# Kernel tuning notes

Measured on AMD Instinct MI355X. Metric: run time of the kernel, lower is better.

## Reference

```python
import jax, jax.numpy as jnp
import numpy as np

NUM_HEADS = 16
HEAD_DIM = 128  # d_out / num_heads = 2048 / 16
WINDOW = 2048   # sliding_window_size


def setup_inputs() -> dict:
    key = jax.random.key(0)
    kx, kq, kk, kv, ko = jax.random.split(key, 5)
    b, s, d = 2, 2048, 2048
    scale = 0.02
    return {
        "x": jax.random.normal(kx, (b, s, d), dtype=jnp.float32),
        "Wq": jax.random.normal(kq, (d, d), dtype=jnp.float32) * scale,
        "Wk": jax.random.normal(kk, (d, d), dtype=jnp.float32) * scale,
        "Wv": jax.random.normal(kv, (d, d), dtype=jnp.float32) * scale,
        "Wo": jax.random.normal(ko, (d, d), dtype=jnp.float32) * scale,
    }


def reference(x, Wq, Wk, Wv, Wo):
    b, s, _ = x.shape
    H, Dh, W = NUM_HEADS, HEAD_DIM, WINDOW

    # qkv projections (no bias), split into heads: [b, s, H, Dh]
    q = (x @ Wq).reshape(b, s, H, Dh)
    k = (x @ Wk).reshape(b, s, H, Dh)
    v = (x @ Wv).reshape(b, s, H, Dh)

    # attn scores: [b, H, q, k]
    scores = jnp.einsum("bqhd,bkhd->bhqk", q, k)

    # sliding-window mask from absolute positions (fresh cache: q_start=k_start=0)
    pos = jnp.arange(s)
    diff = pos[:, None] - pos[None, :]  # q_pos - k_pos
    mask = (diff < 0) | (diff >= W)
    scores = jnp.where(mask[None, None], -jnp.inf, scores)

    attn = jax.nn.softmax(scores / np.sqrt(Dh).astype(np.float32), axis=-1)

    # context: [b, s, H, Dh] -> [b, s, d_out]
    ctx = jnp.einsum("bhqk,bkhd->bqhd", attn, v).reshape(b, s, H * Dh)
    return ctx @ Wo
```

## Files before the change

### kernel.cpp

```cpp
#include <hip/hip_runtime.h>

typedef __bf16 bf16;
typedef __bf16 bf16x4 __attribute__((ext_vector_type(4)));
typedef __bf16 bf16x8 __attribute__((ext_vector_type(8)));
typedef float f32x4 __attribute__((ext_vector_type(4)));

#define B_ 2
#define S_ 2048
#define D_ 2048
#define H_ 16
#define DH_ 128
#define QKVN 6144

__device__ __forceinline__ void async_load16(const bf16* g, bf16* l) {
    __builtin_amdgcn_global_load_lds((const __attribute__((address_space(1))) void*)g,
                                     (__attribute__((address_space(3))) void*)l, 16, 0, 0);
}

__device__ __forceinline__ unsigned int bf16_bits(float x) {
    bf16 h = (bf16)x;
    return (unsigned int)__builtin_bit_cast(unsigned short, h);
}

__global__ __launch_bounds__(256) void cvt_kernel(const float* __restrict__ src,
                                                  bf16* __restrict__ dst) {
    size_t i = (size_t)blockIdx.x * 256 + threadIdx.x;
    const float4* s = (const float4*)src;
    float4 a = s[2 * i], b = s[2 * i + 1];
    bf16x8 o;
    o[0] = (bf16)a.x; o[1] = (bf16)a.y; o[2] = (bf16)a.z; o[3] = (bf16)a.w;
    o[4] = (bf16)b.x; o[5] = (bf16)b.y; o[6] = (bf16)b.z; o[7] = (bf16)b.w;
    *(bf16x8*)(dst + 8 * i) = o;
}

__global__ __launch_bounds__(256) void wtrans_kernel(const float* __restrict__ Wq,
                                                     const float* __restrict__ Wk,
                                                     const float* __restrict__ Wv,
                                                     const float* __restrict__ Wo,
                                                     bf16* __restrict__ WqkvT,
                                                     bf16* __restrict__ WoT) {
    __shared__ unsigned int tile[64][65];
    int z = blockIdx.z;
    const float* src = (z == 0) ? Wq : (z == 1) ? Wk : (z == 2) ? Wv : Wo;
    bf16* dst = (z < 3) ? (WqkvT + (size_t)z * D_ * D_) : WoT;
    int r0 = blockIdx.y * 64, c0 = blockIdx.x * 64;
    int t = threadIdx.x;
    int tr = t >> 4, tc4 = (t & 15) * 4;
#pragma unroll
    for (int it = 0; it < 4; ++it) {
        int r = it * 16 + tr;
        float4 v = *(const float4*)(src + (size_t)(r0 + r) * D_ + c0 + tc4);
        tile[r][tc4 + 0] = bf16_bits(v.x);
        tile[r][tc4 + 1] = bf16_bits(v.y);
        tile[r][tc4 + 2] = bf16_bits(v.z);
        tile[r][tc4 + 3] = bf16_bits(v.w);
    }
    __syncthreads();
#pragma unroll
    for (int it = 0; it < 4; ++it) {
        int a = it * 16 + tr;
        unsigned u0 = tile[tc4 + 0][a], u1 = tile[tc4 + 1][a];
        unsigned u2 = tile[tc4 + 2][a], u3 = tile[tc4 + 3][a];
        uint2 v;
        v.x = (u0 & 0xffffu) | (u1 << 16);
        v.y = (u2 & 0xffffu) | (u3 << 16);
        *(uint2*)(dst + (size_t)(c0 + a) * D_ + r0 + tc4) = v;
    }
}

__global__ __launch_bounds__(256) void vtrans_kernel(const bf16* __restrict__ qkv,
                                                     bf16* __restrict__ vt) {
    __shared__ unsigned int tile[64][65];
    int bh = blockIdx.z;
    int b = bh >> 4, h = bh & 15;
    int s0 = blockIdx.x * 64, d0 = blockIdx.y * 64;
    int t = threadIdx.x, tr = t >> 4, tc4 = (t & 15) * 4;
#pragma unroll
    for (int it = 0; it < 4; ++it) {
        int r = it * 16 + tr;
        uint2 v = *(const uint2*)(qkv + (size_t)(b * S_ + s0 + r) * QKVN + 2 * D_ + h * DH_ + d0 + tc4);
        tile[r][tc4 + 0] = v.x & 0xffffu;
        tile[r][tc4 + 1] = v.x >> 16;
        tile[r][tc4 + 2] = v.y & 0xffffu;
        tile[r][tc4 + 3] = v.y >> 16;
    }
    __syncthreads();
#pragma unroll
    for (int it = 0; it < 4; ++it) {
        int a = it * 16 + tr;
        unsigned u0 = tile[tc4 + 0][a], u1 = tile[tc4 + 1][a];
        unsigned u2 = tile[tc4 + 2][a], u3 = tile[tc4 + 3][a];
        uint2 v;
        v.x = (u0 & 0xffffu) | (u1 << 16);
        v.y = (u2 & 0xffffu) | (u3 << 16);
        *(uint2*)(vt + (size_t)bh * DH_ * S_ + (size_t)(d0 + a) * S_ + s0 + tc4) = v;
    }
}

template <typename CT>
__global__ __launch_bounds__(256) void gemm_bt(const bf16* __restrict__ A,
                                               const bf16* __restrict__ Bt,
                                               CT* __restrict__ C,
                                               int M, int N, int K) {
    __shared__ __align__(16) bf16 As[128 * 32];
    __shared__ __align__(16) bf16 Bs[128 * 32];
    int t = threadIdx.x;
    int w = t >> 6, l = t & 63;
    int quad = l >> 4, lr = l & 15;
    int wr = w >> 1, wc = w & 1;
    size_t m0 = (size_t)blockIdx.y * 128, n0 = (size_t)blockIdx.x * 128;
    int srow = l >> 2, scol = (l & 3) * 8;

    f32x4 acc[4][4];
#pragma unroll
    for (int i = 0; i < 4; ++i)
#pragma unroll
        for (int j = 0; j < 4; ++j) acc[i][j] = (f32x4){0.f, 0.f, 0.f, 0.f};

    for (int k0 = 0; k0 < K; k0 += 32) {
        __syncthreads();
#pragma unroll
        for (int i = 0; i < 2; ++i) {
            int c = w * 2 + i;
            async_load16(A + (m0 + c * 16 + srow) * (size_t)K + k0 + scol, As + c * 512);
            async_load16(Bt + (n0 + c * 16 + srow) * (size_t)K + k0 + scol, Bs + c * 512);
        }
        asm volatile("s_waitcnt vmcnt(0)" ::: "memory");
        __syncthreads();
        bf16x8 af[4], bfr[4];
#pragma unroll
        for (int i = 0; i < 4; ++i) af[i] = *(const bf16x8*)(As + (wr * 64 + i * 16 + lr) * 32 + quad * 8);
#pragma unroll
        for (int j = 0; j < 4; ++j) bfr[j] = *(const bf16x8*)(Bs + (wc * 64 + j * 16 + lr) * 32 + quad * 8);
#pragma unroll
        for (int i = 0; i < 4; ++i)
#pragma unroll
            for (int j = 0; j < 4; ++j)
                acc[i][j] = __builtin_amdgcn_mfma_f32_16x16x32_bf16(af[i], bfr[j], acc[i][j], 0, 0, 0);
    }

    size_t bm = m0 + wr * 64 + quad * 4;
    size_t bn = n0 + wc * 64 + lr;
#pragma unroll
    for (int i = 0; i < 4; ++i)
#pragma unroll
        for (int j = 0; j < 4; ++j)
#pragma unroll
            for (int r = 0; r < 4; ++r)
                C[(bm + i * 16 + r) * (size_t)N + bn + j * 16] = (CT)acc[i][j][r];
}

__global__ __launch_bounds__(128) void attn_kernel(const bf16* __restrict__ qkv,
                                                   const bf16* __restrict__ vt,
                                                   bf16* __restrict__ ctx) {
    __shared__ __align__(16) bf16 Ks[2][64 * 128];
    __shared__ __align__(16) bf16 Vts[2][128 * 64];
    __shared__ __align__(16) bf16 Ps[2][32][68];

    int y = blockIdx.y;
    int p = blockIdx.x;
    int b = y >> 4, h = y & 15;
    int t = threadIdx.x, w = t >> 6, l = t & 63;
    int quad = l >> 4, lr = l & 15;

    const bf16* qbase = qkv + (size_t)b * S_ * QKVN + h * DH_;
    const bf16* kbase = qbase + D_;
    const bf16* vbase = vt + (size_t)y * DH_ * S_;

    const int qtA = p, qtB = 31 - p;
    const int nA = p + 1;

    auto stage = [&](int kt, int bi) {
#pragma unroll
        for (int ii = 0; ii < 8; ++ii) {
            int i = 8 * w + ii;
            int row = 4 * i + (l >> 4);
            int cl = (l & 15) ^ (row & 7);
            async_load16(kbase + (size_t)(kt * 64 + row) * QKVN + cl * 8, Ks[bi] + i * 512);
        }
#pragma unroll
        for (int ii = 0; ii < 8; ++ii) {
            int i = 8 * w + ii;
            int dh = 8 * i + (l >> 3);
            int cl = (l & 7) ^ (dh & 7);
            async_load16(vbase + (size_t)dh * S_ + kt * 64 + cl * 8, Vts[bi] + i * 512);
        }
    };

    const float sc2 = 0.12751745f;

    int qt = qtA, q0 = qt * 64;
    bf16x8 qf[2][4];
    auto loadQ = [&]() {
#pragma unroll
        for (int g = 0; g < 2; ++g)
#pragma unroll
            for (int kk = 0; kk < 4; ++kk) {
                bf16x8 raw = *(const bf16x8*)(qbase + (size_t)(q0 + w * 32 + g * 16 + lr) * QKVN + kk * 32 + quad * 8);
#pragma unroll
                for (int e = 0; e < 8; ++e) qf[g][kk][e] = (bf16)((float)raw[e] * sc2);
            }
    };
    loadQ();

    float L_r[2][4];
    f32x4 o[2][8];
#pragma unroll
    for (int g = 0; g < 2; ++g) {
#pragma unroll
        for (int r = 0; r < 4; ++r) L_r[g][r] = 0.f;
#pragma unroll
        for (int nt = 0; nt < 8; ++nt) o[g][nt] = (f32x4){0.f, 0.f, 0.f, 0.f};
    }

    auto epilogue = [&](int q0e) {
#pragma unroll
        for (int g = 0; g < 2; ++g) {
#pragma unroll
            for (int d = 1; d < 16; d <<= 1)
#pragma unroll
                for (int r = 0; r < 4; ++r) L_r[g][r] += __shfl_xor(L_r[g][r], d, 64);
#pragma unroll
            for (int r = 0; r < 4; ++r) {
                float inv = __builtin_amdgcn_rcpf(L_r[g][r]);
                int q = q0e + w * 32 + g * 16 + quad * 4 + r;
#pragma unroll
                for (int nt = 0; nt < 8; ++nt)
                    ctx[(size_t)(b * S_ + q) * D_ + h * DH_ + nt * 16 + lr] = (bf16)(o[g][nt][r] * inv);
            }
        }
    };

    stage(0, 0);

    for (int it = 0; it < 33; ++it) {
        int buf = it & 1;
        asm volatile("s_waitcnt vmcnt(0)" ::: "memory");
        __syncthreads();
        if (it + 1 < 33) {
            int nit = it + 1;
            int nkt = (nit < nA) ? nit : (nit - nA);
            stage(nkt, buf ^ 1);
        }
        int kt = (it < nA) ? it : (it - nA);

        f32x4 s[2][4];
#pragma unroll
        for (int g = 0; g < 2; ++g)
#pragma unroll
            for (int jt = 0; jt < 4; ++jt) s[g][jt] = (f32x4){0.f, 0.f, 0.f, 0.f};
#pragma unroll
        for (int kk = 0; kk < 4; ++kk)
#pragma unroll
            for (int jt = 0; jt < 4; ++jt) {
                bf16x8 kf = *(const bf16x8*)(Ks[buf] + (jt * 16 + lr) * 128 + ((4 * kk + quad) ^ (lr & 7)) * 8);
                s[0][jt] = __builtin_amdgcn_mfma_f32_16x16x32_bf16(qf[0][kk], kf, s[0][jt], 0, 0, 0);
                s[1][jt] = __builtin_amdgcn_mfma_f32_16x16x32_bf16(qf[1][kk], kf, s[1][jt], 0, 0, 0);
            }

        bool diag = (kt == qt);
#pragma unroll
        for (int g = 0; g < 2; ++g) {
#pragma unroll
            for (int jt = 0; jt < 4; ++jt) {
                int keyi = jt * 16 + lr;
#pragma unroll
                for (int r = 0; r < 4; ++r) {
                    float s2 = s[g][jt][r];
                    if (diag && keyi > w * 32 + g * 16 + quad * 4 + r) s2 = -3.0e38f;
                    float pv = __builtin_amdgcn_exp2f(s2);
                    s[g][jt][r] = pv;
                    L_r[g][r] += pv;
                }
            }
#pragma unroll
            for (int jt = 0; jt < 4; ++jt)
#pragma unroll
                for (int r = 0; r < 4; ++r)
                    Ps[w][g * 16 + quad * 4 + r][jt * 16 + lr] = (bf16)s[g][jt][r];
        }
        asm volatile("s_waitcnt lgkmcnt(0)" ::: "memory");

#pragma unroll
        for (int ks = 0; ks < 2; ++ks) {
            bf16x8 pf[2];
#pragma unroll
            for (int g = 0; g < 2; ++g) {
                const bf16* pp = &Ps[w][g * 16 + lr][ks * 32 + quad * 8];
                bf16x4 lo = *(const bf16x4*)pp;
                bf16x4 hi = *(const bf16x4*)(pp + 4);
                pf[g] = __builtin_shufflevector(lo, hi, 0, 1, 2, 3, 4, 5, 6, 7);
            }
#pragma unroll
            for (int nt = 0; nt < 8; ++nt) {
                bf16x8 vf = *(const bf16x8*)(Vts[buf] + (nt * 16 + lr) * 64 + ((4 * ks + quad) ^ (lr & 7)) * 8);
                o[0][nt] = __builtin_amdgcn_mfma_f32_16x16x32_bf16(pf[0], vf, o[0][nt], 0, 0, 0);
                o[1][nt] = __builtin_amdgcn_mfma_f32_16x16x32_bf16(pf[1], vf, o[1][nt], 0, 0, 0);
            }
        }

        if (it == nA - 1) {
            epilogue(q0);
            qt = qtB;
            q0 = qt * 64;
            loadQ();
#pragma unroll
            for (int g = 0; g < 2; ++g) {
#pragma unroll
                for (int r = 0; r < 4; ++r) L_r[g][r] = 0.f;
#pragma unroll
                for (int nt = 0; nt < 8; ++nt) o[g][nt] = (f32x4){0.f, 0.f, 0.f, 0.f};
            }
        }
    }

    epilogue(q0);
}

extern "C" void kernel_launch(void* const* d_in, const int* in_sizes, int n_in,
                              void* d_out, int out_size, void* d_ws, size_t ws_size,
                              hipStream_t stream) {
    const float* x  = (const float*)d_in[0];
    const float* Wq = (const float*)d_in[1];
    const float* Wk = (const float*)d_in[2];
    const float* Wv = (const float*)d_in[3];
    const float* Wo = (const float*)d_in[4];
    float* out = (float*)d_out;

    char* ws = (char*)d_ws;
    bf16* WqkvT = (bf16*)(ws);
    bf16* WoT   = (bf16*)(ws + 25165824);
    bf16* qkv   = (bf16*)(ws + 33554432);
    bf16* vt    = (bf16*)(ws + 83886080);
    bf16* ctx   = (bf16*)(ws + 100663296);
    bf16* xb    = (bf16*)(ws + 117440512);

    cvt_kernel<<<4096, 256, 0, stream>>>(x, xb);
    wtrans_kernel<<<dim3(32, 32, 4), 256, 0, stream>>>(Wq, Wk, Wv, Wo, WqkvT, WoT);
    gemm_bt<bf16><<<dim3(48, 32), 256, 0, stream>>>(xb, WqkvT, qkv, B_ * S_, QKVN, D_);
    vtrans_kernel<<<dim3(32, 2, 32), 256, 0, stream>>>(qkv, vt);
    attn_kernel<<<dim3(16, 32), 128, 0, stream>>>(qkv, vt, ctx);
    gemm_bt<float><<<dim3(16, 32), 256, 0, stream>>>(ctx, WoT, out, B_ * S_, D_, D_);
}
```

Before: 417.4 us.

## Add specialized 256x256 tiled QKV GEMM with swizzled LDS and interleaved prefetch

Replaces the generic gemm_bt for the QKV projection with a dedicated 512-thread kernel computing 256x256 output tiles. It uses XOR-swizzled LDS to avoid bank conflicts, double-buffered async global-to-LDS loads interleaved with four MFMA quarter-steps, a block-index swizzle for L2 locality, and s_setprio around MFMA bursts. The goal is higher operand reuse and better overlap of loads and compute. The cost is larger shared memory use (128KB per block), many barriers, and hand-tuned waitcnt sequencing that has to be exactly right.

```diff
diff --git a/kernel.cpp b/kernel.cpp
--- a/kernel.cpp
+++ b/kernel.cpp
@@ -150,6 +150,172 @@
                 C[(bm + i * 16 + r) * (size_t)N + bn + j * 16] = (CT)acc[i][j][r];
 }
 
+#define QK_K 2048
+#define QK_N 6144
+
+__device__ __forceinline__ bf16x8 lds_frag(const bf16* tile, int row, int colByte) {
+    int off = row * 128 + (colByte ^ (((row >> 2) & 1) << 5));
+    return *(const bf16x8*)((const char*)tile + off);
+}
+
+template <int MH, int NH>
+__device__ __forceinline__ void mmaq8(f32x4 (&acc)[8][4], const bf16x8 (&afr)[4][2],
+                                      const bf16x8 (&bf)[2][2]) {
+    __builtin_amdgcn_s_setprio(1);
+#pragma unroll
+    for (int i = 0; i < 4; ++i)
+#pragma unroll
+        for (int j = 0; j < 2; ++j)
+#pragma unroll
+            for (int kk = 0; kk < 2; ++kk)
+                acc[MH * 4 + i][NH * 2 + j] = __builtin_amdgcn_mfma_f32_16x16x32_bf16(
+                    afr[i][kk], bf[j][kk], acc[MH * 4 + i][NH * 2 + j], 0, 0, 0);
+    __builtin_amdgcn_s_setprio(0);
+}
+
+__global__ __launch_bounds__(512, 2) void gemm_qkv(const bf16* __restrict__ A,
+                                                   const bf16* __restrict__ Bt,
+                                                   bf16* __restrict__ C) {
+    __shared__ __align__(16) bf16 As[2][256 * 64];
+    __shared__ __align__(16) bf16 Bs[2][256 * 64];
+
+    int t = threadIdx.x;
+    int wid = t >> 6, lane = t & 63;
+    int quad = lane >> 4, lr = lane & 15;
+    int wr = wid >> 2, wn = wid & 3;
+
+    int bid = blockIdx.x;
+    int swz = (bid & 7) * 48 + (bid >> 3);
+    int tn = swz >> 4, tm = swz & 15;
+    size_t m0 = (size_t)tm * 256, n0 = (size_t)tn * 256;
+
+    int row_r[2], c8s_r[2];
+#pragma unroll
+    for (int r = 0; r < 2; ++r) {
+        int idx = r * 512 + t;
+        row_r[r] = idx >> 3;
+        c8s_r[r] = (idx & 7) ^ (((row_r[r] >> 2) & 1) << 1);
+    }
+
+    auto stA = [&](int kt, int bufi, int h) {
+#pragma unroll
+        for (int r = 0; r < 2; ++r)
+            async_load16(A + (m0 + h * 128 + row_r[r]) * (size_t)QK_K + kt * 64 + c8s_r[r] * 8,
+                         &As[bufi][(h * 1024 + r * 512 + wid * 64) * 8]);
+    };
+    auto stB = [&](int kt, int bufi, int h) {
+#pragma unroll
+        for (int r = 0; r < 2; ++r)
+            async_load16(Bt + (n0 + h * 128 + row_r[r]) * (size_t)QK_K + kt * 64 + c8s_r[r] * 8,
+                         &Bs[bufi][(h * 1024 + r * 512 + wid * 64) * 8]);
+    };
+
+    f32x4 acc[8][4];
+#pragma unroll
+    for (int i = 0; i < 8; ++i)
+#pragma unroll
+        for (int j = 0; j < 4; ++j) acc[i][j] = (f32x4){0.f, 0.f, 0.f, 0.f};
+
+    bf16x8 afr[4][2], bf0[2][2], bf1[2][2];
+
+    auto readA = [&](int bufi, int mh) {
+#pragma unroll
+        for (int i = 0; i < 4; ++i)
+#pragma unroll
+            for (int kk = 0; kk < 2; ++kk)
+                afr[i][kk] = lds_frag(As[bufi], mh * 128 + wr * 64 + i * 16 + lr, kk * 64 + quad * 16);
+    };
+    auto readB = [&](int bufi, int nh, bf16x8 (&bf)[2][2]) {
+#pragma unroll
+        for (int j = 0; j < 2; ++j)
+#pragma unroll
+            for (int kk = 0; kk < 2; ++kk)
+                bf[j][kk] = lds_frag(Bs[bufi], nh * 128 + wn * 32 + j * 16 + lr, kk * 64 + quad * 16);
+    };
+
+    stA(0, 0, 0);
+    stB(0, 0, 0);
+    stB(0, 0, 1);
+    stA(0, 0, 1);
+    asm volatile("s_waitcnt vmcnt(4)" ::: "memory");
+    __builtin_amdgcn_s_barrier();
+
+    const int NKT = QK_K / 64;
+    for (int kt = 0; kt < NKT - 1; ++kt) {
+        int cb = kt & 1, nb = cb ^ 1;
+        readA(cb, 0);
+        readB(cb, 0, bf0);
+        stA(kt + 1, nb, 0);
+        asm volatile("s_waitcnt vmcnt(4)" ::: "memory");
+        __builtin_amdgcn_s_barrier();
+        asm volatile("s_waitcnt lgkmcnt(0)" ::: "memory");
+        __builtin_amdgcn_sched_barrier(0);
+        mmaq8<0, 0>(acc, afr, bf0);
+        __builtin_amdgcn_s_barrier();
+        readB(cb, 1, bf1);
+        stB(kt + 1, nb, 0);
+        asm volatile("s_waitcnt vmcnt(4)" ::: "memory");
+        __builtin_amdgcn_s_barrier();
+        asm volatile("s_waitcnt lgkmcnt(0)" ::: "memory");
+        __builtin_amdgcn_sched_barrier(0);
+        mmaq8<0, 1>(acc, afr, bf1);
+        __builtin_amdgcn_s_barrier();
+        readA(cb, 1);
+        stB(kt + 1, nb, 1);
+        __builtin_amdgcn_s_barrier();
+        asm volatile("s_waitcnt lgkmcnt(0)" ::: "memory");
+        __builtin_amdgcn_sched_barrier(0);
+        mmaq8<1, 0>(acc, afr, bf0);
+        __builtin_amdgcn_s_barrier();
+        stA(kt + 1, nb, 1);
+        asm volatile("s_waitcnt vmcnt(4)" ::: "memory");
+        __builtin_amdgcn_s_barrier();
+        mmaq8<1, 1>(acc, afr, bf1);
+        __builtin_amdgcn_s_barrier();
+    }
+
+    {
+        int cb = (NKT - 1) & 1;
+        readA(cb, 0);
+        readB(cb, 0, bf0);
+        asm volatile("s_waitcnt vmcnt(2)" ::: "memory");
+        __builtin_amdgcn_s_barrier();
+        asm volatile("s_waitcnt lgkmcnt(0)" ::: "memory");
+        __builtin_amdgcn_sched_barrier(0);
+        mmaq8<0, 0>(acc, afr, bf0);
+        __builtin_amdgcn_s_barrier();
+        readB(cb, 1, bf1);
+        asm volatile("s_waitcnt vmcnt(0)" ::: "memory");
+        __builtin_amdgcn_s_barrier();
+        asm volatile("s_waitcnt lgkmcnt(0)" ::: "memory");
+        __builtin_amdgcn_sched_barrier(0);
+        mmaq8<0, 1>(acc, afr, bf1);
+        __builtin_amdgcn_s_barrier();
+        readA(cb, 1);
+        __builtin_amdgcn_s_barrier();
+        asm volatile("s_waitcnt lgkmcnt(0)" ::: "memory");
+        __builtin_amdgcn_sched_barrier(0);
+        mmaq8<1, 0>(acc, afr, bf0);
+        __builtin_amdgcn_s_barrier();
+        mmaq8<1, 1>(acc, afr, bf1);
+    }
+
+#pragma unroll
+    for (int mh = 0; mh < 2; ++mh)
+#pragma unroll
+        for (int i = 0; i < 4; ++i)
+#pragma unroll
+            for (int nh = 0; nh < 2; ++nh)
+#pragma unroll
+                for (int j = 0; j < 2; ++j)
+#pragma unroll
+                    for (int r = 0; r < 4; ++r) {
+                        size_t row = m0 + mh * 128 + wr * 64 + i * 16 + quad * 4 + r;
+                        size_t col = n0 + nh * 128 + wn * 32 + j * 16 + lr;
+                        C[row * QK_N + col] = (bf16)acc[mh * 4 + i][nh * 2 + j][r];
+                    }
+}
+
 __global__ __launch_bounds__(128) void attn_kernel(const bf16* __restrict__ qkv,
                                                    const bf16* __restrict__ vt,
                                                    bf16* __restrict__ ctx) {
@@ -337,7 +503,7 @@
 
     cvt_kernel<<<4096, 256, 0, stream>>>(x, xb);
     wtrans_kernel<<<dim3(32, 32, 4), 256, 0, stream>>>(Wq, Wk, Wv, Wo, WqkvT, WoT);
-    gemm_bt<bf16><<<dim3(48, 32), 256, 0, stream>>>(xb, WqkvT, qkv, B_ * S_, QKVN, D_);
+    gemm_qkv<<<dim3(384), 512, 0, stream>>>(xb, WqkvT, qkv);
     vtrans_kernel<<<dim3(32, 2, 32), 256, 0, stream>>>(qkv, vt);
     attn_kernel<<<dim3(16, 32), 128, 0, stream>>>(qkv, vt, ctx);
     gemm_bt<float><<<dim3(16, 32), 256, 0, stream>>>(ctx, WoT, out, B_ * S_, D_, D_);
```

Measured after the change: 431.7 us. 1.03x slower.
